# Kernel optimization log

Measured on AMD Instinct MI355X. Metric: run time of the kernel, lower is better.

The kernel has to match this reference:

```python
import jax, jax.numpy as jnp
import numpy as np

B, D, K, L = 16384, 255, 4, 16  # batch, destinations, tunnels/dst, outgoing links
T = D * K                        # total tunnels = 1020
EPS = 1e-8


def setup_inputs() -> dict:
    key = jax.random.key(0)
    k1, k2, k3, k4, k5 = jax.random.split(key, 5)
    pred_ratios = jax.random.uniform(k1, (B, T), dtype=jnp.float32)
    demands = jax.random.uniform(k2, (B, D), dtype=jnp.float32) * 100.0
    current_link_utils = jax.random.uniform(k3, (B, L), dtype=jnp.float32)
    link_capacities = jax.random.uniform(k4, (L,), dtype=jnp.float32) * 900.0 + 100.0
    tunnel_to_link = jax.random.randint(k5, (T,), 0, L, dtype=jnp.int32)
    return {
        "pred_ratios": pred_ratios,
        "demands": demands,
        "current_link_utils": current_link_utils,
        "link_capacities": link_capacities,
        "tunnel_to_link": tunnel_to_link,
    }


def reference(pred_ratios, demands, current_link_utils, link_capacities, tunnel_to_link):
    # Equal group sizes: destination d owns tunnels [d*K, (d+1)*K)
    Tn = pred_ratios.shape[1]
    Dn = demands.shape[1]
    Kn = Tn // Dn
    Ln = link_capacities.shape[0]
    # tunnel_traffic[b, t] = demand[b, dst(t)] * ratio[b, t]
    tunnel_traffic = pred_ratios * jnp.repeat(demands, Kn, axis=1)  # [B, T]
    # scatter-add tunnels into links, expressed as a dense [T, L] one-hot GEMM
    onehot = jax.nn.one_hot(tunnel_to_link, Ln, dtype=pred_ratios.dtype)  # [T, L]
    node_link_traffic = tunnel_traffic @ onehot  # [B, L]
    node_link_util = node_link_traffic / (link_capacities[None, :] + EPS)
    variance_loss = jnp.var(node_link_util, axis=1, ddof=1).mean()  # torch.var is unbiased
    congestion_penalty = (node_link_util * current_link_utils).sum(axis=1).mean()
    max_util_loss = node_link_util.max(axis=1).mean()
    return 0.3 * variance_loss + 0.5 * congestion_penalty + 0.2 * max_util_loss
```

## Files before the change

### kernel.cpp

```cpp
#include <hip/hip_runtime.h>

constexpr int T_TUN = 1020;
constexpr int D_DST = 255;
constexpr int L_LNK = 16;
constexpr float EPS = 1e-8f;
constexpr int ROWS_PER_BLOCK = 8;

__device__ __forceinline__ float read_lane_f(float v, int l) {
  return __builtin_bit_cast(float,
      __builtin_amdgcn_readlane(__builtin_bit_cast(int, v), l));
}

__global__ __launch_bounds__(256) void rowloss_kernel(
    const float* __restrict__ pred,
    const float* __restrict__ demands,
    const float* __restrict__ cur,
    const float* __restrict__ caps,
    const int*   __restrict__ t2l,
    float* __restrict__ partials)
{
  const int tid  = threadIdx.x;
  const int lane = tid & 63;
  const int w    = tid >> 6;

  __shared__ float privA_all[4][L_LNK * 64];
  __shared__ float privB_all[4][L_LNK * 64];
  __shared__ float wacc[4];
  float* pa = privA_all[w];
  float* pb = privB_all[w];

  const int b16 = lane & 15;
  const int g   = lane >> 4;
  const float capinv = 1.0f / (caps[b16] + EPS);

  int off[4][4];
  bool dv[4];
#pragma unroll
  for (int j = 0; j < 4; ++j) {
    const int d = lane + 64 * j;
    dv[j] = (d < D_DST);
    const int dd = dv[j] ? d : 0;
    const int4 lk = ((const int4*)t2l)[dd];
    off[j][0] = lk.x * 64 + lane;
    off[j][1] = lk.y * 64 + lane;
    off[j][2] = lk.z * 64 + lane;
    off[j][3] = lk.w * 64 + lane;
  }

  const int row0 = blockIdx.x * ROWS_PER_BLOCK + w * 2;

  float4 r4[2][4];
  float  dm[2][4];
  float  mycur[2];
#pragma unroll
  for (int r = 0; r < 2; ++r) {
    const int b = row0 + r;
    const float4* prow = (const float4*)(pred + (size_t)b * T_TUN);
    const float*  drow = demands + (size_t)b * D_DST;
    mycur[r] = cur[(size_t)b * L_LNK + b16];
#pragma unroll
    for (int j = 0; j < 4; ++j) {
      const int d = lane + 64 * j;
      if (dv[j]) { r4[r][j] = prow[d]; dm[r][j] = drow[d]; }
    }
  }

  {
    const float4 z = make_float4(0.f, 0.f, 0.f, 0.f);
    float4* pza = (float4*)pa;
    float4* pzb = (float4*)pb;
#pragma unroll
    for (int i = 0; i < 4; ++i) { pza[lane + 64 * i] = z; pzb[lane + 64 * i] = z; }
  }

  __builtin_amdgcn_wave_barrier();

#pragma unroll
  for (int j = 0; j < 4; ++j) {
    if (!dv[j]) continue;
    const float4 vA = r4[0][j];
    const float  dA = dm[0][j];
    const float4 vB = r4[1][j];
    const float  dB = dm[1][j];
    pa[off[j][0]] += vA.x * dA;
    pb[off[j][0]] += vB.x * dB;
    pa[off[j][1]] += vA.y * dA;
    pb[off[j][1]] += vB.y * dB;
    pa[off[j][2]] += vA.z * dA;
    pb[off[j][2]] += vB.z * dB;
    pa[off[j][3]] += vA.w * dA;
    pb[off[j][3]] += vB.w * dB;
  }

  __builtin_amdgcn_wave_barrier();

  float csA = 0.0f, csB = 0.0f;
  {
    const float4* prA = (const float4*)(pa + b16 * 64 + 16 * g);
    const float4* prB = (const float4*)(pb + b16 * 64 + 16 * g);
#pragma unroll
    for (int q = 0; q < 4; ++q) {
      const float4 a = prA[q];
      csA += a.x + a.y + a.z + a.w;
      const float4 b = prB[q];
      csB += b.x + b.y + b.z + b.w;
    }
  }
  csA += __shfl_xor(csA, 16, 64);
  csA += __shfl_xor(csA, 32, 64);
  csB += __shfl_xor(csB, 16, 64);
  csB += __shfl_xor(csB, 32, 64);

  const float uA = csA * capinv;
  const float uB = csB * capinv;

  float valA = (g == 0) ? uA : (g == 1) ? (uA * uA)
             : (g == 2) ? (uA * mycur[0]) : uA;
  float valB = (g == 0) ? uB : (g == 1) ? (uB * uB)
             : (g == 2) ? (uB * mycur[1]) : uB;
#pragma unroll
  for (int m = 1; m < 16; m <<= 1) {
    const float oA  = __shfl_xor(valA, m, 64);
    const float smA = valA + oA;
    const float mmA = fmaxf(valA, oA);
    valA = (g == 3) ? mmA : smA;
    const float oB  = __shfl_xor(valB, m, 64);
    const float smB = valB + oB;
    const float mmB = fmaxf(valB, oB);
    valB = (g == 3) ? mmB : smB;
  }
  float acc = 0.0f;
  {
    const float s1 = read_lane_f(valA, 0);
    const float s2 = read_lane_f(valA, 16);
    const float s3 = read_lane_f(valA, 32);
    const float mx = read_lane_f(valA, 48);
    const float var = (s2 - s1 * s1 * (1.0f / 16.0f)) * (1.0f / 15.0f);
    acc += 0.3f * var + 0.5f * s3 + 0.2f * mx;
  }
  {
    const float s1 = read_lane_f(valB, 0);
    const float s2 = read_lane_f(valB, 16);
    const float s3 = read_lane_f(valB, 32);
    const float mx = read_lane_f(valB, 48);
    const float var = (s2 - s1 * s1 * (1.0f / 16.0f)) * (1.0f / 15.0f);
    acc += 0.3f * var + 0.5f * s3 + 0.2f * mx;
  }

  if (lane == 0) wacc[w] = acc;
  __syncthreads();
  if (tid == 0) partials[blockIdx.x] = wacc[0] + wacc[1] + wacc[2] + wacc[3];
}

__global__ __launch_bounds__(256) void reduce_kernel(
    const float* __restrict__ partials, int n, float* __restrict__ out, float invB)
{
  __shared__ float s[256];
  const int tid = threadIdx.x;
  const float4* p4 = (const float4*)partials;
  const int n4 = n >> 2;
  float a = 0.0f;
  for (int i = tid; i < n4; i += 256) {
    const float4 v = p4[i];
    a += v.x + v.y + v.z + v.w;
  }
  s[tid] = a;
  __syncthreads();
  for (int st = 128; st > 0; st >>= 1) {
    if (tid < st) s[tid] += s[tid + st];
    __syncthreads();
  }
  if (tid == 0) out[0] = s[0] * invB;
}

extern "C" void kernel_launch(void* const* d_in, const int* in_sizes, int n_in,
                              void* d_out, int out_size, void* d_ws, size_t ws_size,
                              hipStream_t stream) {
  const float* pred    = (const float*)d_in[0];
  const float* demands = (const float*)d_in[1];
  const float* cur     = (const float*)d_in[2];
  const float* caps    = (const float*)d_in[3];
  const int*   t2l     = (const int*)d_in[4];
  float* out = (float*)d_out;

  const int L = in_sizes[3];
  const int B = in_sizes[2] / L;

  const int grid = B / ROWS_PER_BLOCK;
  float* partials = (float*)d_ws;

  rowloss_kernel<<<grid, 256, 0, stream>>>(pred, demands, cur, caps, t2l, partials);
  reduce_kernel<<<1, 256, 0, stream>>>(partials, grid, out, 1.0f / (float)B);
}
```

Measured before the change: 107.3 us.

## Make row kernel persistent with double-buffered row prefetch and interleaved float2 bins

The grid is cut from one block per 8 rows to a fixed 512 blocks, each looping over 4 iterations. The next iteration's rows are prefetched into registers while the current ones are binned, to hide global-load latency. The two per-row LDS histograms are merged into one interleaved float2 array, so each bin update is a single 64-bit LDS read-modify-write. The bin readback is rotated per lane to spread bank accesses. Doubling the register buffers raises VGPR pressure and may lower occupancy, and fewer blocks means less parallelism for hiding latency.

```diff
diff --git a/kernel.cpp b/kernel.cpp
--- a/kernel.cpp
+++ b/kernel.cpp
@@ -4,7 +4,10 @@
 constexpr int D_DST = 255;
 constexpr int L_LNK = 16;
 constexpr float EPS = 1e-8f;
-constexpr int ROWS_PER_BLOCK = 8;
+
+constexpr int GRID_BLOCKS = 512;
+constexpr int ROWS_PER_ITER = 8;
+constexpr int NITER = 16384 / (GRID_BLOCKS * ROWS_PER_ITER);
 
 __device__ __forceinline__ float read_lane_f(float v, int l) {
   return __builtin_bit_cast(float,
@@ -23,11 +26,9 @@
   const int lane = tid & 63;
   const int w    = tid >> 6;
 
-  __shared__ float privA_all[4][L_LNK * 64];
-  __shared__ float privB_all[4][L_LNK * 64];
+  __shared__ float2 bins_all[4][L_LNK * 64];
   __shared__ float wacc[4];
-  float* pa = privA_all[w];
-  float* pb = privB_all[w];
+  float2* pb = bins_all[w];
 
   const int b16 = lane & 15;
   const int g   = lane >> 4;
@@ -47,104 +48,113 @@
     off[j][3] = lk.w * 64 + lane;
   }
 
-  const int row0 = blockIdx.x * ROWS_PER_BLOCK + w * 2;
-
-  float4 r4[2][4];
-  float  dm[2][4];
-  float  mycur[2];
-#pragma unroll
-  for (int r = 0; r < 2; ++r) {
-    const int b = row0 + r;
-    const float4* prow = (const float4*)(pred + (size_t)b * T_TUN);
-    const float*  drow = demands + (size_t)b * D_DST;
-    mycur[r] = cur[(size_t)b * L_LNK + b16];
+  const int rowbase = blockIdx.x * (NITER * ROWS_PER_ITER) + w * 2;
+
+  float4 r4[2][2][4];
+  float  dm[2][2][4];
+  float  cur2[2][2];
+
+  auto loadp = [&](int t, int buf) {
+#pragma unroll
+    for (int r = 0; r < 2; ++r) {
+      const int b = rowbase + t * ROWS_PER_ITER + r;
+      const float4* prow = (const float4*)(pred + (size_t)b * T_TUN);
+      const float*  drow = demands + (size_t)b * D_DST;
+      cur2[buf][r] = cur[(size_t)b * L_LNK + b16];
+#pragma unroll
+      for (int j = 0; j < 4; ++j) {
+        const int d = lane + 64 * j;
+        if (dv[j]) { r4[buf][r][j] = prow[d]; dm[buf][r][j] = drow[d]; }
+      }
+    }
+  };
+
+  loadp(0, 0);
+
+  float acc = 0.0f;
+
+#pragma unroll
+  for (int t = 0; t < NITER; ++t) {
+    const int buf = t & 1;
+    if (t + 1 < NITER) loadp(t + 1, buf ^ 1);
+
+    __builtin_amdgcn_wave_barrier();
+
+    {
+      const float4 z = make_float4(0.f, 0.f, 0.f, 0.f);
+      float4* pz = (float4*)pb;
+#pragma unroll
+      for (int i = 0; i < 8; ++i) pz[lane + 64 * i] = z;
+    }
+
+    __builtin_amdgcn_wave_barrier();
+
 #pragma unroll
     for (int j = 0; j < 4; ++j) {
-      const int d = lane + 64 * j;
-      if (dv[j]) { r4[r][j] = prow[d]; dm[r][j] = drow[d]; }
-    }
-  }
-
-  {
-    const float4 z = make_float4(0.f, 0.f, 0.f, 0.f);
-    float4* pza = (float4*)pa;
-    float4* pzb = (float4*)pb;
-#pragma unroll
-    for (int i = 0; i < 4; ++i) { pza[lane + 64 * i] = z; pzb[lane + 64 * i] = z; }
-  }
-
-  __builtin_amdgcn_wave_barrier();
-
-#pragma unroll
-  for (int j = 0; j < 4; ++j) {
-    if (!dv[j]) continue;
-    const float4 vA = r4[0][j];
-    const float  dA = dm[0][j];
-    const float4 vB = r4[1][j];
-    const float  dB = dm[1][j];
-    pa[off[j][0]] += vA.x * dA;
-    pb[off[j][0]] += vB.x * dB;
-    pa[off[j][1]] += vA.y * dA;
-    pb[off[j][1]] += vB.y * dB;
-    pa[off[j][2]] += vA.z * dA;
-    pb[off[j][2]] += vB.z * dB;
-    pa[off[j][3]] += vA.w * dA;
-    pb[off[j][3]] += vB.w * dB;
-  }
-
-  __builtin_amdgcn_wave_barrier();
-
-  float csA = 0.0f, csB = 0.0f;
-  {
-    const float4* prA = (const float4*)(pa + b16 * 64 + 16 * g);
-    const float4* prB = (const float4*)(pb + b16 * 64 + 16 * g);
-#pragma unroll
-    for (int q = 0; q < 4; ++q) {
-      const float4 a = prA[q];
-      csA += a.x + a.y + a.z + a.w;
-      const float4 b = prB[q];
-      csB += b.x + b.y + b.z + b.w;
-    }
-  }
-  csA += __shfl_xor(csA, 16, 64);
-  csA += __shfl_xor(csA, 32, 64);
-  csB += __shfl_xor(csB, 16, 64);
-  csB += __shfl_xor(csB, 32, 64);
-
-  const float uA = csA * capinv;
-  const float uB = csB * capinv;
-
-  float valA = (g == 0) ? uA : (g == 1) ? (uA * uA)
-             : (g == 2) ? (uA * mycur[0]) : uA;
-  float valB = (g == 0) ? uB : (g == 1) ? (uB * uB)
-             : (g == 2) ? (uB * mycur[1]) : uB;
-#pragma unroll
-  for (int m = 1; m < 16; m <<= 1) {
-    const float oA  = __shfl_xor(valA, m, 64);
-    const float smA = valA + oA;
-    const float mmA = fmaxf(valA, oA);
-    valA = (g == 3) ? mmA : smA;
-    const float oB  = __shfl_xor(valB, m, 64);
-    const float smB = valB + oB;
-    const float mmB = fmaxf(valB, oB);
-    valB = (g == 3) ? mmB : smB;
-  }
-  float acc = 0.0f;
-  {
-    const float s1 = read_lane_f(valA, 0);
-    const float s2 = read_lane_f(valA, 16);
-    const float s3 = read_lane_f(valA, 32);
-    const float mx = read_lane_f(valA, 48);
-    const float var = (s2 - s1 * s1 * (1.0f / 16.0f)) * (1.0f / 15.0f);
-    acc += 0.3f * var + 0.5f * s3 + 0.2f * mx;
-  }
-  {
-    const float s1 = read_lane_f(valB, 0);
-    const float s2 = read_lane_f(valB, 16);
-    const float s3 = read_lane_f(valB, 32);
-    const float mx = read_lane_f(valB, 48);
-    const float var = (s2 - s1 * s1 * (1.0f / 16.0f)) * (1.0f / 15.0f);
-    acc += 0.3f * var + 0.5f * s3 + 0.2f * mx;
+      if (!dv[j]) continue;
+      const float4 vA = r4[buf][0][j]; const float dA = dm[buf][0][j];
+      const float4 vB = r4[buf][1][j]; const float dB = dm[buf][1][j];
+      { const int o = off[j][0]; float2 s = pb[o];
+        s.x = fmaf(vA.x, dA, s.x); s.y = fmaf(vB.x, dB, s.y); pb[o] = s; }
+      { const int o = off[j][1]; float2 s = pb[o];
+        s.x = fmaf(vA.y, dA, s.x); s.y = fmaf(vB.y, dB, s.y); pb[o] = s; }
+      { const int o = off[j][2]; float2 s = pb[o];
+        s.x = fmaf(vA.z, dA, s.x); s.y = fmaf(vB.z, dB, s.y); pb[o] = s; }
+      { const int o = off[j][3]; float2 s = pb[o];
+        s.x = fmaf(vA.w, dA, s.x); s.y = fmaf(vB.w, dB, s.y); pb[o] = s; }
+    }
+
+    __builtin_amdgcn_wave_barrier();
+
+    float csA = 0.0f, csB = 0.0f;
+    {
+      const float4* pr = (const float4*)(pb + b16 * 64 + 16 * g);
+#pragma unroll
+      for (int jj = 0; jj < 8; ++jj) {
+        const float4 v = pr[(jj + b16) & 7];
+        csA += v.x + v.z;
+        csB += v.y + v.w;
+      }
+    }
+    csA += __shfl_xor(csA, 16, 64);
+    csA += __shfl_xor(csA, 32, 64);
+    csB += __shfl_xor(csB, 16, 64);
+    csB += __shfl_xor(csB, 32, 64);
+
+    const float uA = csA * capinv;
+    const float uB = csB * capinv;
+
+    float valA = (g == 0) ? uA : (g == 1) ? (uA * uA)
+               : (g == 2) ? (uA * cur2[buf][0]) : uA;
+    float valB = (g == 0) ? uB : (g == 1) ? (uB * uB)
+               : (g == 2) ? (uB * cur2[buf][1]) : uB;
+#pragma unroll
+    for (int m = 1; m < 16; m <<= 1) {
+      const float oA  = __shfl_xor(valA, m, 64);
+      const float smA = valA + oA;
+      const float mmA = fmaxf(valA, oA);
+      valA = (g == 3) ? mmA : smA;
+      const float oB  = __shfl_xor(valB, m, 64);
+      const float smB = valB + oB;
+      const float mmB = fmaxf(valB, oB);
+      valB = (g == 3) ? mmB : smB;
+    }
+    {
+      const float s1 = read_lane_f(valA, 0);
+      const float s2 = read_lane_f(valA, 16);
+      const float s3 = read_lane_f(valA, 32);
+      const float mx = read_lane_f(valA, 48);
+      const float var = (s2 - s1 * s1 * (1.0f / 16.0f)) * (1.0f / 15.0f);
+      acc += 0.3f * var + 0.5f * s3 + 0.2f * mx;
+    }
+    {
+      const float s1 = read_lane_f(valB, 0);
+      const float s2 = read_lane_f(valB, 16);
+      const float s3 = read_lane_f(valB, 32);
+      const float mx = read_lane_f(valB, 48);
+      const float var = (s2 - s1 * s1 * (1.0f / 16.0f)) * (1.0f / 15.0f);
+      acc += 0.3f * var + 0.5f * s3 + 0.2f * mx;
+    }
   }
 
   if (lane == 0) wacc[w] = acc;
@@ -186,7 +196,7 @@
   const int L = in_sizes[3];
   const int B = in_sizes[2] / L;
 
-  const int grid = B / ROWS_PER_BLOCK;
+  const int grid = GRID_BLOCKS;
   float* partials = (float*)d_ws;
 
   rowloss_kernel<<<grid, 256, 0, stream>>>(pred, demands, cur, caps, t2l, partials);
```

Result: no change. 109.3 us (+1.9%).
